# Kernel tuning notes

Measured on AMD Instinct MI355X. Metric: run time of the kernel, lower is better.

Reference implementation:

```python
import jax, jax.numpy as jnp
import numpy as np

# Mamba2 dims (defaults: expand=2, d_state=128, d_conv=4, ngroups=1)
D_MODEL = 1024
HEADDIM = 64
D_STATE = 128
D_CONV = 4
D_INNER = 2 * D_MODEL            # 2048
NHEADS = D_INNER // HEADDIM      # 32
CONV_DIM = D_INNER + 2 * D_STATE # 2304
D_IN_PROJ = 2 * D_INNER + 2 * D_STATE + NHEADS  # 4384
EPS = 1e-5


def setup_inputs() -> dict:
    key = jax.random.key(0)
    ks = jax.random.split(key, 12)
    B, L = 4, 2048
    inp = {}
    inp['query'] = jax.random.normal(ks[0], (B, L, D_MODEL), jnp.float32)
    inp['key'] = jax.random.normal(ks[1], (B, L, D_MODEL), jnp.float32)
    inp['value'] = jax.random.normal(ks[2], (B, L, D_MODEL), jnp.float32)
    # parameters (Mamba2-style init)
    inp['in_proj_w'] = jax.random.normal(ks[3], (D_IN_PROJ, D_MODEL), jnp.float32) * (D_MODEL ** -0.5)
    inp['conv_w'] = jax.random.normal(ks[4], (CONV_DIM, D_CONV), jnp.float32) * (D_CONV ** -0.5)
    inp['conv_b'] = jnp.zeros((CONV_DIM,), jnp.float32)
    # dt init: softplus^{-1}(dt) with dt ~ U[1e-3, 1e-1]
    dt = jnp.exp(jax.random.uniform(ks[5], (NHEADS,)) * (np.log(0.1) - np.log(1e-3)) + np.log(1e-3))
    inp['dt_bias'] = dt + jnp.log(-jnp.expm1(-dt))
    # A ~ U[1, 16], A_log = log(A)
    inp['A_log'] = jnp.log(jax.random.uniform(ks[6], (NHEADS,), minval=1.0, maxval=16.0))
    inp['D'] = jnp.ones((NHEADS,), jnp.float32)
    inp['norm_w'] = jnp.ones((D_INNER,), jnp.float32)
    inp['out_proj_w'] = jax.random.normal(ks[7], (D_MODEL, D_INNER), jnp.float32) * (D_INNER ** -0.5)
    return inp


def _mamba2_forward(u, in_proj_w, conv_w, conv_b, dt_bias, A_log, D, norm_w, out_proj_w):
    b, l, _ = u.shape
    zxbcdt = jnp.einsum('bld,ed->ble', u, in_proj_w)  # (b,l,D_IN_PROJ)
    z = zxbcdt[..., :D_INNER]
    xBC = zxbcdt[..., D_INNER:D_INNER + CONV_DIM]
    dt = jax.nn.softplus(zxbcdt[..., -NHEADS:] + dt_bias)  # (b,l,h)
    # depthwise causal conv1d over time, kernel D_CONV, + silu
    xBC_pad = jnp.pad(xBC, ((0, 0), (D_CONV - 1, 0), (0, 0)))
    conv = conv_b
    for k in range(D_CONV):
        conv = conv + xBC_pad[:, k:k + l, :] * conv_w[:, k]
    xBC = jax.nn.silu(conv)
    x = xBC[..., :D_INNER].reshape(b, l, NHEADS, HEADDIM)   # (b,l,h,p)
    Bm = xBC[..., D_INNER:D_INNER + D_STATE]                # (b,l,n) ngroups=1
    Cm = xBC[..., D_INNER + D_STATE:]                       # (b,l,n)
    A = -jnp.exp(A_log)                                      # (h,)
    dA = jnp.exp(dt * A)                                     # (b,l,h)

    def step(h, inputs):
        dA_t, dt_t, x_t, B_t, C_t = inputs  # (b,h),(b,h),(b,h,p),(b,n),(b,n)
        h = h * dA_t[:, :, None, None] + (dt_t[:, :, None, None] * x_t[..., None]) * B_t[:, None, None, :]
        y = jnp.einsum('bhpn,bn->bhp', h, C_t)
        return h, y

    h0 = jnp.zeros((b, NHEADS, HEADDIM, D_STATE), u.dtype)
    xs = (dA.transpose(1, 0, 2), dt.transpose(1, 0, 2), x.transpose(1, 0, 2, 3),
          Bm.transpose(1, 0, 2), Cm.transpose(1, 0, 2))
    _, ys = jax.lax.scan(step, h0, xs)
    y = ys.transpose(1, 0, 2, 3) + x * D[None, None, :, None]  # (b,l,h,p)
    y = y.reshape(b, l, D_INNER)
    # RMSNormGated (norm_before_gate=False): norm(y * silu(z)) * w
    y = y * jax.nn.silu(z)
    y = y * jax.lax.rsqrt(jnp.mean(y * y, axis=-1, keepdims=True) + EPS) * norm_w
    return jnp.einsum('ble,de->bld', y, out_proj_w)


def reference(query, key, value, in_proj_w, conv_w, conv_b, dt_bias, A_log, D, norm_w, out_proj_w):
    # wrapper ignores key/value; returns mamba(query) (cache pass-through omitted)
    return _mamba2_forward(query, in_proj_w, conv_w, conv_b, dt_bias, A_log, D, norm_w, out_proj_w)
```

## Files before the change

### kernel.cpp

```cpp
#include <hip/hip_runtime.h>
#include <hip/hip_bf16.h>


typedef __attribute__((ext_vector_type(8))) short bf16x8;
typedef __attribute__((ext_vector_type(4))) float f32x4;

static constexpr int B_ = 4;
static constexpr int L_ = 2048;
static constexpr int NROWS = B_ * L_;
static constexpr int DMODEL = 1024;
static constexpr int DINNER = 2048;
static constexpr int NH = 32;
static constexpr int DSTATE = 128;
static constexpr int CONVDIM = DINNER + 2 * DSTATE;
static constexpr int DINPROJ = 2 * DINNER + 2 * DSTATE + NH;
static constexpr int Q_ = 64;
static constexpr int NCHUNK = L_ / Q_;

__device__ __forceinline__ unsigned pk_bf16(float a, float b) {
  unsigned ua = __builtin_bit_cast(unsigned, a);
  unsigned ub = __builtin_bit_cast(unsigned, b);
  ua = (ua + 0x7FFFu + ((ua >> 16) & 1u)) >> 16;
  ub = (ub + 0x7FFFu + ((ub >> 16) & 1u)) >> 16;
  return (ua & 0xFFFFu) | (ub << 16);
}
__device__ __forceinline__ unsigned short bf16_of(float a) {
  unsigned ua = __builtin_bit_cast(unsigned, a);
  return (unsigned short)((ua + 0x7FFFu + ((ua >> 16) & 1u)) >> 16);
}
__device__ __forceinline__ float f_of_bf16(unsigned short s) {
  return __builtin_bit_cast(float, (unsigned)s << 16);
}
__device__ __forceinline__ unsigned short* state_slot(unsigned short* lo,
                                                      unsigned short* hi,
                                                      int bh, int c) {
  int i = bh * NCHUNK + c;
  return (i < 2048) ? lo + (size_t)i * 8192 : hi + (size_t)(i - 2048) * 8192;
}

__global__ __launch_bounds__(256) void cast4_kernel(const float* __restrict__ in,
                                                    unsigned short* __restrict__ out) {
  int i = blockIdx.x * 256 + threadIdx.x;
  float4 v = ((const float4*)in)[i];
  ((uint2*)out)[i] = make_uint2(pk_bf16(v.x, v.y), pk_bf16(v.z, v.w));
}

template <bool C_BF16>
__global__ __launch_bounds__(256) void gemm_lds_kernel(
    const unsigned short* __restrict__ A, const unsigned short* __restrict__ Bw,
    void* __restrict__ Cp, int M, int N, int K, int lda, int ldb, int ldc) {
  __shared__ unsigned short sA[128 * 32];
  __shared__ unsigned short sB[128 * 32];
  const int tid = threadIdx.x;
  const int w = tid >> 6;
  const int lane = tid & 63;
  const int m0 = blockIdx.y * 128;
  const int n0 = blockIdx.x * 128;
  const int wm = (w >> 1) * 64;
  const int wn = (w & 1) * 64;
  const int lr = lane >> 2;
  const int lc8 = (lane & 3) * 8;

  f32x4 acc[4][4];
#pragma unroll
  for (int i = 0; i < 4; ++i)
#pragma unroll
    for (int j = 0; j < 4; ++j) acc[i][j] = f32x4{0.f, 0.f, 0.f, 0.f};

  auto ldsA = (__attribute__((address_space(3))) unsigned short*)sA;
  auto ldsB = (__attribute__((address_space(3))) unsigned short*)sB;

  for (int k0 = 0; k0 < K; k0 += 32) {
#pragma unroll
    for (int s = 0; s < 2; ++s) {
      int row = w * 32 + s * 16;
      __builtin_amdgcn_global_load_lds(
          (const __attribute__((address_space(1))) void*)(A + (size_t)(m0 + row + lr) * lda + k0 + lc8),
          (__attribute__((address_space(3))) void*)(ldsA + row * 32), 16, 0, 0);
      __builtin_amdgcn_global_load_lds(
          (const __attribute__((address_space(1))) void*)(Bw + (size_t)(n0 + row + lr) * ldb + k0 + lc8),
          (__attribute__((address_space(3))) void*)(ldsB + row * 32), 16, 0, 0);
    }
    __syncthreads();
    const int k8 = (lane >> 4) * 8;
    const int r15 = lane & 15;
    bf16x8 af[4], bfr[4];
#pragma unroll
    for (int i = 0; i < 4; ++i)
      af[i] = *(const bf16x8*)(sA + (wm + i * 16 + r15) * 32 + k8);
#pragma unroll
    for (int j = 0; j < 4; ++j)
      bfr[j] = *(const bf16x8*)(sB + (wn + j * 16 + r15) * 32 + k8);
#pragma unroll
    for (int i = 0; i < 4; ++i)
#pragma unroll
      for (int j = 0; j < 4; ++j)
        acc[i][j] = __builtin_amdgcn_mfma_f32_16x16x32_bf16(af[i], bfr[j], acc[i][j], 0, 0, 0);
    __syncthreads();
  }

  const int rr = (lane >> 4) * 4;
  const int cc = lane & 15;
#pragma unroll
  for (int i = 0; i < 4; ++i) {
#pragma unroll
    for (int j = 0; j < 4; ++j) {
      int gcol = n0 + wn + j * 16 + cc;
      if (gcol < N) {
#pragma unroll
        for (int r = 0; r < 4; ++r) {
          size_t grow = (size_t)(m0 + wm + i * 16 + rr + r);
          if constexpr (C_BF16)
            ((unsigned short*)Cp)[grow * ldc + gcol] = bf16_of(acc[i][j][r]);
          else
            ((float*)Cp)[grow * ldc + gcol] = acc[i][j][r];
        }
      }
    }
  }
}

__global__ __launch_bounds__(256) void conv_kernel(const unsigned short* __restrict__ zx,
                                                   const float* __restrict__ conv_w,
                                                   const float* __restrict__ conv_b,
                                                   unsigned short* __restrict__ xbc) {
  int c = blockIdx.x * 256 + threadIdx.x;
  int row = blockIdx.y;
  int l = row & (L_ - 1);
  float acc = conv_b[c];
#pragma unroll
  for (int k = 0; k < 4; ++k) {
    int ll = l + k - 3;
    if (ll >= 0)
      acc = fmaf(f_of_bf16(zx[(size_t)(row + k - 3) * DINPROJ + DINNER + c]),
                 conv_w[c * 4 + k], acc);
  }
  acc = acc / (1.f + __expf(-acc));
  xbc[(size_t)row * CONVDIM + c] = bf16_of(acc);
}

__global__ __launch_bounds__(256) void dt_kernel(const unsigned short* __restrict__ zx,
                                                 const float* __restrict__ dt_bias,
                                                 float* __restrict__ dtv) {
  int i = blockIdx.x * 256 + threadIdx.x;
  int hh = i & (NH - 1);
  int row = i >> 5;
  float x = f_of_bf16(zx[(size_t)row * DINPROJ + DINNER + CONVDIM + hh]) + dt_bias[hh];
  dtv[i] = (x > 20.f) ? x : log1pf(__expf(x));
}

__global__ __launch_bounds__(256) void ssd_passA(unsigned short* __restrict__ xbc,
                                                 const float* __restrict__ dtv,
                                                 const float* __restrict__ A_log,
                                                 const float* __restrict__ Dvec,
                                                 unsigned short* __restrict__ st_lo,
                                                 unsigned short* __restrict__ st_hi) {
  const int bid = blockIdx.x;
  const int h = bid & 31;
  const int c = (bid >> 5) & 31;
  const int b = bid >> 10;
  const int bh = b * 32 + h;
  const int tid = threadIdx.x;
  const int w = tid >> 6;
  const int lane = tid & 63;
  const int quad = lane >> 4;
  const int c15 = lane & 15;

  __shared__ unsigned short sXt[64 * 72];
  __shared__ unsigned short sBq[64 * 136];
  __shared__ unsigned short sCB[128 * 72];
  __shared__ float sdt[64], scs[64], sg[64];

  const float A = -__expf(A_log[h]);
  const float Dh = Dvec[h];
  const int r0 = b * L_ + c * Q_;

  if (w == 0) {
    float v = dtv[(size_t)(r0 + lane) * NH + h];
    sdt[lane] = v;
    float s = v;
#pragma unroll
    for (int off = 1; off < 64; off <<= 1) {
      float t = __shfl_up(s, off, 64);
      if (lane >= off) s += t;
    }
    scs[lane] = s;
    float T = __shfl(s, 63, 64);
    sg[lane] = __expf(A * (T - s)) * v;
  }
  for (int e = tid; e < 512; e += 256) {
    int t = e & 63, pb = e >> 6;
    uint4 v = *(const uint4*)&xbc[(size_t)(r0 + t) * CONVDIM + h * 64 + pb * 8];
    const unsigned short* sv = (const unsigned short*)&v;
#pragma unroll
    for (int j = 0; j < 8; ++j) sXt[(pb * 8 + j) * 72 + t] = sv[j];
  }
  for (int e = tid; e < 1024; e += 256) {
    int s = e >> 4, ch = e & 15;
    size_t roff = (size_t)(r0 + s) * CONVDIM + DINNER;
    *(uint4*)&sBq[s * 136 + ch * 8] = *(const uint4*)&xbc[roff + ch * 8];
    *(uint4*)&sCB[s * 136 + ch * 8] = *(const uint4*)&xbc[roff + DSTATE + ch * 8];
  }
  __syncthreads();

  const int wt = w >> 1, wx = w & 1;
  f32x4 sacc[2][2];
#pragma unroll
  for (int i = 0; i < 2; ++i)
#pragma unroll
    for (int j = 0; j < 2; ++j) sacc[i][j] = f32x4{0.f, 0.f, 0.f, 0.f};
#pragma unroll
  for (int kk = 0; kk < 4; ++kk) {
    int k8 = quad * 8 + kk * 32;
    bf16x8 a0 = *(const bf16x8*)&sCB[(wt * 32 + c15) * 136 + k8];
    bf16x8 a1 = *(const bf16x8*)&sCB[(wt * 32 + 16 + c15) * 136 + k8];
    bf16x8 b0 = *(const bf16x8*)&sBq[(wx * 32 + c15) * 136 + k8];
    bf16x8 b1 = *(const bf16x8*)&sBq[(wx * 32 + 16 + c15) * 136 + k8];
    sacc[0][0] = __builtin_amdgcn_mfma_f32_16x16x32_bf16(a0, b0, sacc[0][0], 0, 0, 0);
    sacc[0][1] = __builtin_amdgcn_mfma_f32_16x16x32_bf16(a0, b1, sacc[0][1], 0, 0, 0);
    sacc[1][0] = __builtin_amdgcn_mfma_f32_16x16x32_bf16(a1, b0, sacc[1][0], 0, 0, 0);
    sacc[1][1] = __builtin_amdgcn_mfma_f32_16x16x32_bf16(a1, b1, sacc[1][1], 0, 0, 0);
  }
  __syncthreads();

#pragma unroll
  for (int i = 0; i < 2; ++i)
#pragma unroll
    for (int j = 0; j < 2; ++j) {
      int scol = wx * 32 + j * 16 + c15;
      float css = scs[scol], dts = sdt[scol];
#pragma unroll
      for (int r = 0; r < 4; ++r) {
        int trow = wt * 32 + i * 16 + quad * 4 + r;
        float v = (scol <= trow) ? sacc[i][j][r] * __expf(A * (scs[trow] - css)) * dts : 0.f;
        sBq[trow * 72 + scol] = bf16_of(v);
      }
    }
  for (int e = tid; e < 1024; e += 256) {
    int s = e & 63, nb = e >> 6;
    uint4 v = *(const uint4*)&xbc[(size_t)(r0 + s) * CONVDIM + DINNER + nb * 8];
    float g = sg[s];
    const unsigned short* sv = (const unsigned short*)&v;
#pragma unroll
    for (int j = 0; j < 8; ++j)
      sCB[(nb * 8 + j) * 72 + s] = bf16_of(f_of_bf16(sv[j]) * g);
  }
  __syncthreads();

  f32x4 yacc[2][2];
#pragma unroll
  for (int i = 0; i < 2; ++i)
#pragma unroll
    for (int j = 0; j < 2; ++j) yacc[i][j] = f32x4{0.f, 0.f, 0.f, 0.f};
#pragma unroll
  for (int kk = 0; kk < 2; ++kk) {
    int k8 = quad * 8 + kk * 32;
    bf16x8 a0 = *(const bf16x8*)&sBq[(wt * 32 + c15) * 72 + k8];
    bf16x8 a1 = *(const bf16x8*)&sBq[(wt * 32 + 16 + c15) * 72 + k8];
    bf16x8 b0 = *(const bf16x8*)&sXt[(wx * 32 + c15) * 72 + k8];
    bf16x8 b1 = *(const bf16x8*)&sXt[(wx * 32 + 16 + c15) * 72 + k8];
    yacc[0][0] = __builtin_amdgcn_mfma_f32_16x16x32_bf16(a0, b0, yacc[0][0], 0, 0, 0);
    yacc[0][1] = __builtin_amdgcn_mfma_f32_16x16x32_bf16(a0, b1, yacc[0][1], 0, 0, 0);
    yacc[1][0] = __builtin_amdgcn_mfma_f32_16x16x32_bf16(a1, b0, yacc[1][0], 0, 0, 0);
    yacc[1][1] = __builtin_amdgcn_mfma_f32_16x16x32_bf16(a1, b1, yacc[1][1], 0, 0, 0);
  }
#pragma unroll
  for (int i = 0; i < 2; ++i)
#pragma unroll
    for (int j = 0; j < 2; ++j) {
      int p = wx * 32 + j * 16 + c15;
#pragma unroll
      for (int r = 0; r < 4; ++r) {
        int t = wt * 32 + i * 16 + quad * 4 + r;
        float xv = f_of_bf16(sXt[p * 72 + t]);
        xbc[(size_t)(r0 + t) * CONVDIM + h * 64 + p] = bf16_of(yacc[i][j][r] + Dh * xv);
      }
    }

  f32x4 hacc[2][4];
#pragma unroll
  for (int i = 0; i < 2; ++i)
#pragma unroll
    for (int j = 0; j < 4; ++j) hacc[i][j] = f32x4{0.f, 0.f, 0.f, 0.f};
  const int wp = w >> 1, wn = w & 1;
#pragma unroll
  for (int kk = 0; kk < 2; ++kk) {
    int k8 = quad * 8 + kk * 32;
    bf16x8 a0 = *(const bf16x8*)&sXt[(wp * 32 + c15) * 72 + k8];
    bf16x8 a1 = *(const bf16x8*)&sXt[(wp * 32 + 16 + c15) * 72 + k8];
    bf16x8 bfr[4];
#pragma unroll
    for (int j = 0; j < 4; ++j)
      bfr[j] = *(const bf16x8*)&sCB[(wn * 64 + j * 16 + c15) * 72 + k8];
#pragma unroll
    for (int j = 0; j < 4; ++j) {
      hacc[0][j] = __builtin_amdgcn_mfma_f32_16x16x32_bf16(a0, bfr[j], hacc[0][j], 0, 0, 0);
      hacc[1][j] = __builtin_amdgcn_mfma_f32_16x16x32_bf16(a1, bfr[j], hacc[1][j], 0, 0, 0);
    }
  }
  unsigned short* slot = state_slot(st_lo, st_hi, bh, c);
#pragma unroll
  for (int i = 0; i < 2; ++i)
#pragma unroll
    for (int j = 0; j < 4; ++j)
#pragma unroll
      for (int r = 0; r < 4; ++r) {
        int p = wp * 32 + i * 16 + quad * 4 + r;
        int n = wn * 64 + j * 16 + c15;
        slot[p * 128 + n] = bf16_of(hacc[i][j][r]);
      }
}

__global__ __launch_bounds__(256) void ssd_passB(const float* __restrict__ dtv,
                                                 const float* __restrict__ A_log,
                                                 unsigned short* __restrict__ st_lo,
                                                 unsigned short* __restrict__ st_hi) {
  const int bh = blockIdx.x >> 1;
  const int ph = blockIdx.x & 1;
  const int h = bh & 31;
  const int b = bh >> 5;
  const int tid = threadIdx.x;
  __shared__ float sd[NCHUNK];
  const float A = -__expf(A_log[h]);
  if (tid < NCHUNK) {
    float s = 0.f;
    const float* dp = dtv + (size_t)(b * L_ + tid * Q_) * NH + h;
    for (int i = 0; i < Q_; ++i) s += dp[(size_t)i * NH];
    sd[tid] = __expf(A * s);
  }
  __syncthreads();
  float hreg[16];
#pragma unroll
  for (int k = 0; k < 16; ++k) hreg[k] = 0.f;
  const size_t eoff = (size_t)ph * 4096 + (size_t)tid * 16;
  for (int c = 0; c < NCHUNK; ++c) {
    unsigned short* sp = state_slot(st_lo, st_hi, bh, c) + eoff;
    uint4 t0 = ((const uint4*)sp)[0];
    uint4 t1 = ((const uint4*)sp)[1];
    unsigned o[8];
#pragma unroll
    for (int k = 0; k < 8; ++k) o[k] = pk_bf16(hreg[2 * k], hreg[2 * k + 1]);
    ((uint4*)sp)[0] = make_uint4(o[0], o[1], o[2], o[3]);
    ((uint4*)sp)[1] = make_uint4(o[4], o[5], o[6], o[7]);
    float d = sd[c];
    const unsigned short* tv0 = (const unsigned short*)&t0;
    const unsigned short* tv1 = (const unsigned short*)&t1;
#pragma unroll
    for (int k = 0; k < 8; ++k) hreg[k] = d * hreg[k] + f_of_bf16(tv0[k]);
#pragma unroll
    for (int k = 0; k < 8; ++k) hreg[8 + k] = d * hreg[8 + k] + f_of_bf16(tv1[k]);
  }
}

__global__ __launch_bounds__(256) void ssd_passC(unsigned short* __restrict__ xbc,
                                                 const float* __restrict__ dtv,
                                                 const float* __restrict__ A_log,
                                                 const unsigned short* __restrict__ st_lo,
                                                 const unsigned short* __restrict__ st_hi) {
  const int bid = blockIdx.x;
  const int h = bid & 31;
  const int c = (bid >> 5) & 31;
  const int b = bid >> 10;
  const int bh = b * 32 + h;
  const int tid = threadIdx.x;
  const int w = tid >> 6;
  const int lane = tid & 63;
  const int quad = lane >> 4;
  const int c15 = lane & 15;

  __shared__ unsigned short sC[64 * 136];
  __shared__ unsigned short sH[64 * 136];
  __shared__ float srt[64];

  const float A = -__expf(A_log[h]);
  const int r0 = b * L_ + c * Q_;

  if (w == 0) {
    float v = dtv[(size_t)(r0 + lane) * NH + h];
    float s = v;
#pragma unroll
    for (int off = 1; off < 64; off <<= 1) {
      float t = __shfl_up(s, off, 64);
      if (lane >= off) s += t;
    }
    srt[lane] = __expf(A * s);
  }
  const unsigned short* slot =
      state_slot((unsigned short*)st_lo, (unsigned short*)st_hi, bh, c);
  for (int e = tid; e < 1024; e += 256) {
    int s = e >> 4, ch = e & 15;
    *(uint4*)&sC[s * 136 + ch * 8] =
        *(const uint4*)&xbc[(size_t)(r0 + s) * CONVDIM + DINNER + DSTATE + ch * 8];
    *(uint4*)&sH[s * 136 + ch * 8] = *(const uint4*)&slot[s * 128 + ch * 8];
  }
  __syncthreads();

  const int wt = w >> 1, wx = w & 1;
  f32x4 yacc[2][2];
#pragma unroll
  for (int i = 0; i < 2; ++i)
#pragma unroll
    for (int j = 0; j < 2; ++j) yacc[i][j] = f32x4{0.f, 0.f, 0.f, 0.f};
#pragma unroll
  for (int kk = 0; kk < 4; ++kk) {
    int k8 = quad * 8 + kk * 32;
    bf16x8 a0 = *(const bf16x8*)&sC[(wt * 32 + c15) * 136 + k8];
    bf16x8 a1 = *(const bf16x8*)&sC[(wt * 32 + 16 + c15) * 136 + k8];
    bf16x8 b0 = *(const bf16x8*)&sH[(wx * 32 + c15) * 136 + k8];
    bf16x8 b1 = *(const bf16x8*)&sH[(wx * 32 + 16 + c15) * 136 + k8];
    yacc[0][0] = __builtin_amdgcn_mfma_f32_16x16x32_bf16(a0, b0, yacc[0][0], 0, 0, 0);
    yacc[0][1] = __builtin_amdgcn_mfma_f32_16x16x32_bf16(a0, b1, yacc[0][1], 0, 0, 0);
    yacc[1][0] = __builtin_amdgcn_mfma_f32_16x16x32_bf16(a1, b0, yacc[1][0], 0, 0, 0);
    yacc[1][1] = __builtin_amdgcn_mfma_f32_16x16x32_bf16(a1, b1, yacc[1][1], 0, 0, 0);
  }
#pragma unroll
  for (int i = 0; i < 2; ++i)
#pragma unroll
    for (int j = 0; j < 2; ++j) {
      int p = wx * 32 + j * 16 + c15;
#pragma unroll
      for (int r = 0; r < 4; ++r) {
        int t = wt * 32 + i * 16 + quad * 4 + r;
        size_t ga = (size_t)(r0 + t) * CONVDIM + h * 64 + p;
        float v = yacc[i][j][r] * srt[t] + f_of_bf16(xbc[ga]);
        xbc[ga] = bf16_of(v);
      }
    }
}

__global__ __launch_bounds__(256) void norm_kernel(const unsigned short* __restrict__ y_in,
                                                   unsigned short* __restrict__ zxb,
                                                   const float* __restrict__ norm_w) {
  const int row = blockIdx.x;
  const int tid = threadIdx.x;
  float v[8];
  float ss = 0.f;
#pragma unroll
  for (int i = 0; i < 8; ++i) {
    int c = tid + i * 256;
    float yv = f_of_bf16(y_in[(size_t)row * CONVDIM + c]);
    float z = f_of_bf16(zxb[(size_t)row * DINPROJ + c]);
    yv *= z / (1.f + __expf(-z));
    v[i] = yv;
    ss = fmaf(yv, yv, ss);
  }
#pragma unroll
  for (int o = 32; o > 0; o >>= 1) ss += __shfl_down(ss, o, 64);
  __shared__ float sred[4];
  if ((tid & 63) == 0) sred[tid >> 6] = ss;
  __syncthreads();
  float tot = (sred[0] + sred[1]) + (sred[2] + sred[3]);
  float r = rsqrtf(tot * (1.f / (float)DINNER) + 1e-5f);
#pragma unroll
  for (int i = 0; i < 8; ++i) {
    int c = tid + i * 256;
    zxb[(size_t)row * DINPROJ + c] = bf16_of(v[i] * r * norm_w[c]);
  }
}

extern "C" void kernel_launch(void* const* d_in, const int* in_sizes, int n_in,
                              void* d_out, int out_size, void* d_ws, size_t ws_size,
                              hipStream_t stream) {
  (void)in_sizes; (void)n_in; (void)out_size;
  const float* u          = (const float*)d_in[0];
  const float* in_proj_w  = (const float*)d_in[3];
  const float* conv_w     = (const float*)d_in[4];
  const float* conv_b     = (const float*)d_in[5];
  const float* dt_bias    = (const float*)d_in[6];
  const float* A_log      = (const float*)d_in[7];
  const float* Dvec       = (const float*)d_in[8];
  const float* norm_w     = (const float*)d_in[9];
  const float* out_proj_w = (const float*)d_in[10];
  float* out = (float*)d_out;

  constexpr size_t SZ_ZX   = (size_t)NROWS * DINPROJ * 2;
  constexpr size_t SZ_XBC  = (size_t)NROWS * CONVDIM * 2;
  constexpr size_t SZ_DT   = (size_t)NROWS * NH * 4;
  constexpr size_t SZ_SHR  = 33554432;
  constexpr size_t SZ_WOUT = (size_t)DMODEL * DINNER * 2;
  constexpr size_t NEED = SZ_ZX + SZ_XBC + SZ_DT + SZ_SHR + SZ_WOUT;
  if (ws_size < NEED) return;

  char* p = (char*)d_ws;
  unsigned short* zxb  = (unsigned short*)p; p += SZ_ZX;
  unsigned short* xbc  = (unsigned short*)p; p += SZ_XBC;
  float* dtv           = (float*)p;          p += SZ_DT;
  char* shared_reg     = p;                  p += SZ_SHR;
  unsigned short* wout_bf = (unsigned short*)p;

  unsigned short* u_bf   = (unsigned short*)shared_reg;
  unsigned short* win_bf = (unsigned short*)(shared_reg + 16777216);
  unsigned short* st_lo  = (unsigned short*)d_out;
  unsigned short* st_hi  = (unsigned short*)shared_reg;

  cast4_kernel<<<(NROWS * DMODEL) / 1024, 256, 0, stream>>>(u, u_bf);
  cast4_kernel<<<(DINPROJ * DMODEL) / 1024, 256, 0, stream>>>(in_proj_w, win_bf);
  cast4_kernel<<<(DMODEL * DINNER) / 1024, 256, 0, stream>>>(out_proj_w, wout_bf);

  gemm_lds_kernel<true><<<dim3(35, 64), 256, 0, stream>>>(
      u_bf, win_bf, zxb, NROWS, DINPROJ, DMODEL, DMODEL, DMODEL, DINPROJ);
  conv_kernel<<<dim3(9, NROWS), 256, 0, stream>>>(zxb, conv_w, conv_b, xbc);
  dt_kernel<<<(NROWS * NH) / 256, 256, 0, stream>>>(zxb, dt_bias, dtv);

  ssd_passA<<<B_ * NCHUNK * NH, 256, 0, stream>>>(xbc, dtv, A_log, Dvec, st_lo, st_hi);
  ssd_passB<<<B_ * NH * 2, 256, 0, stream>>>(dtv, A_log, st_lo, st_hi);
  ssd_passC<<<B_ * NCHUNK * NH, 256, 0, stream>>>(xbc, dtv, A_log, st_lo, st_hi);

  norm_kernel<<<NROWS, 256, 0, stream>>>(xbc, zxb, norm_w);
  gemm_lds_kernel<false><<<dim3(8, 64), 256, 0, stream>>>(
      zxb, wout_bf, out, NROWS, DMODEL, DINNER, DINPROJ, DINNER, DMODEL);
}
```

Before: 521.1 us.

## Replace GEMM with 256x256-tile, 4-stage LDS-pipelined swizzled kernel

Replaces the 128x128 single-buffer GEMM with a 512-thread kernel that computes 256x256 output tiles. It keeps a 4-stage ring of direct global-to-LDS loads in flight and waits with explicit vmcnt counts, and it XOR-swizzles the LDS columns to avoid bank conflicts. Blocks are remapped so neighbouring tiles land on the same XCD, and MFMA sections are raised in priority. The aim is to hide global load latency and raise data reuse. In exchange it uses about 128KB of LDS, which limits occupancy, and more tile area is wasted on padding past N.

```diff
diff --git a/kernel.cpp b/kernel.cpp
--- a/kernel.cpp
+++ b/kernel.cpp
@@ -45,75 +45,120 @@
   ((uint2*)out)[i] = make_uint2(pk_bf16(v.x, v.y), pk_bf16(v.z, v.w));
 }
 
+#define WAITVM(N) asm volatile("s_waitcnt vmcnt(" #N ")" ::: "memory")
+
 template <bool C_BF16>
-__global__ __launch_bounds__(256) void gemm_lds_kernel(
+__global__ __launch_bounds__(512, 2) void gemm256_kernel(
     const unsigned short* __restrict__ A, const unsigned short* __restrict__ Bw,
     void* __restrict__ Cp, int M, int N, int K, int lda, int ldb, int ldc) {
-  __shared__ unsigned short sA[128 * 32];
-  __shared__ unsigned short sB[128 * 32];
+  (void)M;
+  __shared__ unsigned short sA[4 * 256 * 32];
+  __shared__ unsigned short sB[4 * 256 * 32];
   const int tid = threadIdx.x;
   const int w = tid >> 6;
   const int lane = tid & 63;
-  const int m0 = blockIdx.y * 128;
-  const int n0 = blockIdx.x * 128;
-  const int wm = (w >> 1) * 64;
-  const int wn = (w & 1) * 64;
-  const int lr = lane >> 2;
-  const int lc8 = (lane & 3) * 8;
-
-  f32x4 acc[4][4];
-#pragma unroll
-  for (int i = 0; i < 4; ++i)
+  const int quad = lane >> 4;
+  const int r15 = lane & 15;
+
+  const int NT = gridDim.x;
+  const int nwg = NT * gridDim.y;
+  const int orig = blockIdx.y * NT + blockIdx.x;
+  const int qq = nwg >> 3, rm = nwg & 7;
+  const int xcd = orig & 7, loc = orig >> 3;
+  const int id = (xcd < rm ? xcd * (qq + 1) : rm * (qq + 1) + (xcd - rm) * qq) + loc;
+  const int m0 = (id / NT) << 8;
+  const int n0 = (id % NT) << 8;
+
+  const int wm = w >> 2;
+  const int wn = w & 3;
+
+  const int srow = lane >> 2;
+  const int sch = lane & 3;
+  const int row0 = w * 32 + srow;
+  const int row1 = row0 + 16;
+  const int ca0 = (sch ^ ((row0 >> 1) & 3)) * 8;
+  const int ca1 = (sch ^ ((row1 >> 1) & 3)) * 8;
+  const int nslice = K >> 5;
+
+  f32x4 acc[8][4];
+#pragma unroll
+  for (int i = 0; i < 8; ++i)
 #pragma unroll
     for (int j = 0; j < 4; ++j) acc[i][j] = f32x4{0.f, 0.f, 0.f, 0.f};
 
   auto ldsA = (__attribute__((address_space(3))) unsigned short*)sA;
   auto ldsB = (__attribute__((address_space(3))) unsigned short*)sB;
 
-  for (int k0 = 0; k0 < K; k0 += 32) {
-#pragma unroll
-    for (int s = 0; s < 2; ++s) {
-      int row = w * 32 + s * 16;
-      __builtin_amdgcn_global_load_lds(
-          (const __attribute__((address_space(1))) void*)(A + (size_t)(m0 + row + lr) * lda + k0 + lc8),
-          (__attribute__((address_space(3))) void*)(ldsA + row * 32), 16, 0, 0);
-      __builtin_amdgcn_global_load_lds(
-          (const __attribute__((address_space(1))) void*)(Bw + (size_t)(n0 + row + lr) * ldb + k0 + lc8),
-          (__attribute__((address_space(3))) void*)(ldsB + row * 32), 16, 0, 0);
-    }
-    __syncthreads();
-    const int k8 = (lane >> 4) * 8;
-    const int r15 = lane & 15;
-    bf16x8 af[4], bfr[4];
-#pragma unroll
-    for (int i = 0; i < 4; ++i)
-      af[i] = *(const bf16x8*)(sA + (wm + i * 16 + r15) * 32 + k8);
-#pragma unroll
-    for (int j = 0; j < 4; ++j)
-      bfr[j] = *(const bf16x8*)(sB + (wn + j * 16 + r15) * 32 + k8);
-#pragma unroll
-    for (int i = 0; i < 4; ++i)
-#pragma unroll
-      for (int j = 0; j < 4; ++j)
-        acc[i][j] = __builtin_amdgcn_mfma_f32_16x16x32_bf16(af[i], bfr[j], acc[i][j], 0, 0, 0);
-    __syncthreads();
-  }
-
-  const int rr = (lane >> 4) * 4;
-  const int cc = lane & 15;
-#pragma unroll
-  for (int i = 0; i < 4; ++i) {
+  auto stage = [&](int ks) {
+    const int so = (ks & 3) * 8192 + w * 1024;
+    const unsigned short* ga = A + (size_t)(m0 + row0) * lda + ks * 32;
+    const unsigned short* gb = Bw + (size_t)(n0 + row0) * ldb + ks * 32;
+    __builtin_amdgcn_global_load_lds(
+        (const __attribute__((address_space(1))) void*)(ga + ca0),
+        (__attribute__((address_space(3))) void*)(ldsA + so), 16, 0, 0);
+    __builtin_amdgcn_global_load_lds(
+        (const __attribute__((address_space(1))) void*)(gb + ca0),
+        (__attribute__((address_space(3))) void*)(ldsB + so), 16, 0, 0);
+    __builtin_amdgcn_global_load_lds(
+        (const __attribute__((address_space(1))) void*)(ga + (size_t)16 * lda + ca1),
+        (__attribute__((address_space(3))) void*)(ldsA + so + 512), 16, 0, 0);
+    __builtin_amdgcn_global_load_lds(
+        (const __attribute__((address_space(1))) void*)(gb + (size_t)16 * ldb + ca1),
+        (__attribute__((address_space(3))) void*)(ldsB + so + 512), 16, 0, 0);
+  };
+
+  stage(0);
+  stage(1);
+  stage(2);
+  WAITVM(8);
+  __builtin_amdgcn_s_barrier();
+
+  const int kx = (quad ^ ((r15 >> 1) & 3)) * 8;
+  int s = 0;
+
+#define GPHASE(STAGE_STMT, WTN)                                                \
+  {                                                                            \
+    const unsigned short* pa = sA + (s & 3) * 8192;                            \
+    const unsigned short* pb = sB + (s & 3) * 8192;                            \
+    bf16x8 af[8], bfv[4];                                                      \
+    _Pragma("unroll") for (int i = 0; i < 8; ++i)                              \
+        af[i] = *(const bf16x8*)&pa[(wm * 128 + i * 16 + r15) * 32 + kx];      \
+    _Pragma("unroll") for (int j = 0; j < 4; ++j)                              \
+        bfv[j] = *(const bf16x8*)&pb[(wn * 64 + j * 16 + r15) * 32 + kx];      \
+    STAGE_STMT;                                                                \
+    WAITVM(WTN);                                                               \
+    __builtin_amdgcn_s_barrier();                                              \
+    __builtin_amdgcn_s_setprio(1);                                             \
+    _Pragma("unroll") for (int i = 0; i < 8; ++i)                              \
+        _Pragma("unroll") for (int j = 0; j < 4; ++j)                          \
+            acc[i][j] = __builtin_amdgcn_mfma_f32_16x16x32_bf16(               \
+                af[i], bfv[j], acc[i][j], 0, 0, 0);                            \
+    __builtin_amdgcn_s_setprio(0);                                             \
+    __builtin_amdgcn_s_barrier();                                              \
+  }
+
+  for (; s < nslice - 3; ++s) GPHASE(stage(s + 3), 8);
+  GPHASE((void)0, 4);
+  ++s;
+  GPHASE((void)0, 0);
+  ++s;
+  GPHASE((void)0, 0);
+#undef GPHASE
+
+  const int rq = quad * 4;
+#pragma unroll
+  for (int i = 0; i < 8; ++i) {
 #pragma unroll
     for (int j = 0; j < 4; ++j) {
-      int gcol = n0 + wn + j * 16 + cc;
+      int gcol = n0 + wn * 64 + j * 16 + r15;
       if (gcol < N) {
 #pragma unroll
         for (int r = 0; r < 4; ++r) {
-          size_t grow = (size_t)(m0 + wm + i * 16 + rr + r);
+          size_t grow = (size_t)(m0 + wm * 128 + i * 16 + rq + r);
           if constexpr (C_BF16)
-            ((unsigned short*)Cp)[grow * ldc + gcol] = bf16_of(acc[i][j][r]);
+            ((unsigned short*)Cp)[grow * (size_t)ldc + gcol] = bf16_of(acc[i][j][r]);
           else
-            ((float*)Cp)[grow * ldc + gcol] = acc[i][j][r];
+            ((float*)Cp)[grow * (size_t)ldc + gcol] = acc[i][j][r];
         }
       }
     }
@@ -497,7 +542,7 @@
   cast4_kernel<<<(DINPROJ * DMODEL) / 1024, 256, 0, stream>>>(in_proj_w, win_bf);
   cast4_kernel<<<(DMODEL * DINNER) / 1024, 256, 0, stream>>>(out_proj_w, wout_bf);
 
-  gemm_lds_kernel<true><<<dim3(35, 64), 256, 0, stream>>>(
+  gemm256_kernel<true><<<dim3(18, 32), 512, 0, stream>>>(
       u_bf, win_bf, zxb, NROWS, DINPROJ, DMODEL, DMODEL, DMODEL, DINPROJ);
   conv_kernel<<<dim3(9, NROWS), 256, 0, stream>>>(zxb, conv_w, conv_b, xbc);
   dt_kernel<<<(NROWS * NH) / 256, 256, 0, stream>>>(zxb, dt_bias, dtv);
@@ -507,6 +552,6 @@
   ssd_passC<<<B_ * NCHUNK * NH, 256, 0, stream>>>(xbc, dtv, A_log, st_lo, st_hi);
 
   norm_kernel<<<NROWS, 256, 0, stream>>>(xbc, zxb, norm_w);
-  gemm_lds_kernel<false><<<dim3(8, 64), 256, 0, stream>>>(
+  gemm256_kernel<false><<<dim3(4, 32), 512, 0, stream>>>(
       zxb, wout_bf, out, NROWS, DMODEL, DINNER, DINPROJ, DINNER, DMODEL);
 }
```

Result: faster. 510.3 us (-2.1%).
